# Kernel optimization log

Hardware: AMD Instinct MI355X
Metric: run time of the kernel (lower is better)

## Reference

```python
import jax, jax.numpy as jnp
import numpy as np

N_NODES = 20000
N_EDGES = 320000
NFEAT = 50
ALPHA = 0.2  # leaky relu slope
EPS = 1e-16


def _gat_head(x, src, dst, W, a, concat):
    # x: (N, Fin), W: (Fin, Fout), a: (2*Fout,)
    N = x.shape[0]
    Wh = x @ W                      # (N, Fout)
    Fout = W.shape[1]
    # edge_h @ a == Wh[src] @ a[:Fout] + Wh[dst] @ a[Fout:]
    s_src = Wh @ a[:Fout]           # (N,)
    s_dst = Wh @ a[Fout:]           # (N,)
    e = jax.nn.leaky_relu(s_src[src] + s_dst[dst], negative_slope=ALPHA)  # (E,)
    # segment softmax over incoming edges of each target node
    e_max = jax.ops.segment_max(e, dst, num_segments=N)   # (N,)
    e_exp = jnp.exp(e - e_max[dst])                         # (E,)
    e_sum = jax.ops.segment_sum(e_exp, dst, num_segments=N)
    att = e_exp / (e_sum[dst] + EPS)                        # (E,)
    msg = Wh[src] * att[:, None]                            # (E, Fout)
    h = jax.ops.segment_sum(msg, dst, num_segments=N)       # (N, Fout)
    return jax.nn.elu(h) if concat else h


def _multi_head(x, src, dst, W, a, concat):
    # W: (H, Fin, Fout), a: (H, 2*Fout) -> (H, N, Fout)
    return jax.vmap(_gat_head, in_axes=(None, None, None, 0, 0, None))(x, src, dst, W, a, concat)


def setup_inputs() -> dict:
    key = jax.random.key(0)
    ks = jax.random.split(key, 8)
    x = jax.random.normal(ks[0], (N_NODES, NFEAT), dtype=jnp.float32)
    edge_index = jax.random.randint(ks[1], (2, N_EDGES), 0, N_NODES, dtype=jnp.int64)
    s = 0.1
    W1 = jax.random.normal(ks[2], (4, NFEAT, 256), dtype=jnp.float32) * s
    a1 = jax.random.normal(ks[3], (4, 512), dtype=jnp.float32) * s
    W2 = jax.random.normal(ks[4], (4, 1024, 256), dtype=jnp.float32) * s
    a2 = jax.random.normal(ks[5], (4, 512), dtype=jnp.float32) * s
    W3 = jax.random.normal(ks[6], (6, 1024, 121), dtype=jnp.float32) * s
    a3 = jax.random.normal(ks[7], (6, 242), dtype=jnp.float32) * s
    return {"x": x, "edge_index": edge_index, "W1": W1, "a1": a1, "W2": W2, "a2": a2, "W3": W3, "a3": a3}


def reference(x, edge_index, W1, a1, W2, a2, W3, a3):
    src, dst = edge_index[0], edge_index[1]
    N = x.shape[0]
    # layer 1: 4 heads, concat -> (N, 1024), then elu
    h1 = _multi_head(x, src, dst, W1, a1, True)      # (4, N, 256)
    x1 = jnp.transpose(h1, (1, 0, 2)).reshape(N, -1)  # concat along feature dim
    x1 = jax.nn.elu(x1)
    # layer 2: 4 heads, concat + skip connection, then elu
    h2 = _multi_head(x1, src, dst, W2, a2, True)
    x2 = jnp.transpose(h2, (1, 0, 2)).reshape(N, -1)
    x2 = jax.nn.elu(x2 + x1)
    # layer 3: 6 heads, no concat-elu, mean over heads
    h3 = _multi_head(x2, src, dst, W3, a3, False)     # (6, N, 121)
    x3 = jnp.mean(h3, axis=0)
    return jax.nn.sigmoid(x3)
```

## Files before the change

### kernel.cpp

```cpp
#include <hip/hip_runtime.h>
#include <cstdint>

#define N_NODES 20000
#define N_EDGES 320000
#define ALPHA 0.2f
#define GAT_EPS 1e-16f
#define MPAD 20096
#define RBLK 157
#define RHI 20
#define SCAN_BLKS 80
#define BT_ROWS 1152

typedef __attribute__((ext_vector_type(8))) _Float16 half8;
typedef __attribute__((ext_vector_type(4))) _Float16 half4t;
typedef __attribute__((ext_vector_type(16))) float f32x16;
typedef __attribute__((ext_vector_type(2))) float f32x2;

__device__ __forceinline__ float elu1(float x) { return x > 0.f ? x : __expf(x) - 1.f; }

__device__ __forceinline__ unsigned char f2fp8(float x) {
    return (unsigned char)(__builtin_amdgcn_cvt_pk_fp8_f32(x, 0.f, 0, false) & 0xff);
}

__device__ __forceinline__ void async16(const void* g, void* l) {
    __builtin_amdgcn_global_load_lds(
        (const __attribute__((address_space(1))) unsigned int*)g,
        (__attribute__((address_space(3))) unsigned int*)l, 16, 0, 0);
}

__device__ __forceinline__ float rdlanef(float v, int j) {
    return __int_as_float(__builtin_amdgcn_readlane(__float_as_int(v), j));
}

template <bool HI>
__device__ __forceinline__ f32x2 cvt8(unsigned int u) {
    return __builtin_amdgcn_cvt_pk_f32_fp8((int)u, HI);
}

__global__ void hist_kernel(const int* __restrict__ dst, int* __restrict__ counts, int E) {
    int e = blockIdx.x * blockDim.x + threadIdx.x;
    if (e < E) atomicAdd(&counts[dst[e]], 1);
}

__global__ void scan1_kernel(const int* __restrict__ counts, int* __restrict__ excl,
                             int* __restrict__ partial, int N) {
    __shared__ int sh[256];
    int t = threadIdx.x, b = blockIdx.x;
    int i = b * 256 + t;
    int v = (i < N) ? counts[i] : 0;
    sh[t] = v;
    __syncthreads();
    for (int d = 1; d < 256; d <<= 1) {
        int x = (t >= d) ? sh[t - d] : 0;
        __syncthreads();
        sh[t] += x;
        __syncthreads();
    }
    if (i < N) excl[i] = sh[t] - v;
    if (t == 255) partial[b] = sh[255];
}

__global__ void scan2_kernel(int* __restrict__ partial) {
    __shared__ int sh[128];
    int t = threadIdx.x;
    int v = (t < SCAN_BLKS) ? partial[t] : 0;
    sh[t] = v;
    __syncthreads();
    for (int d = 1; d < 128; d <<= 1) {
        int x = (t >= d) ? sh[t - d] : 0;
        __syncthreads();
        sh[t] += x;
        __syncthreads();
    }
    if (t < SCAN_BLKS) partial[t] = sh[t] - v;
}

__global__ void scan3_kernel(const int* __restrict__ excl, const int* __restrict__ partial,
                             int* __restrict__ rowptr, int* __restrict__ cursor, int N, int E) {
    int t = threadIdx.x, b = blockIdx.x;
    int i = b * 256 + t;
    if (i < N) {
        int v = excl[i] + partial[b];
        rowptr[i] = v;
        cursor[i] = v;
    }
    if (i == 0) rowptr[N] = E;
}

__global__ void scatter_kernel(const int* __restrict__ src, const int* __restrict__ dst,
                               int* __restrict__ cursor, int* __restrict__ esrc, int E) {
    int e = blockIdx.x * blockDim.x + threadIdx.x;
    if (e < E) {
        int p = atomicAdd(&cursor[dst[e]], 1);
        esrc[p] = src[e];
    }
}

__global__ void pack_x16(const float* __restrict__ x, _Float16* __restrict__ A) {
    int idx = blockIdx.x * 256 + threadIdx.x;
    int r = idx >> 6, c = idx & 63;
    float v = (r < N_NODES && c < 50) ? x[r * 50 + c] : 0.f;
    A[idx] = (_Float16)v;
}

__global__ void pack_bt1(const float* __restrict__ W, _Float16* __restrict__ Bt) {
    int idx = blockIdx.x * 256 + threadIdx.x;
    int c = idx >> 6, k = idx & 63;
    int h = c >> 8, f = c & 255;
    float v = (k < 50) ? W[((size_t)h * 50 + k) * 256 + f] : 0.f;
    Bt[idx] = (_Float16)v;
}

__global__ void pack_bt16(const float* __restrict__ W, _Float16* __restrict__ Bt,
                          int F, int Fpad, int Ctot) {
    int c = blockIdx.y;
    int k = blockIdx.x * blockDim.x + threadIdx.x;
    float v = 0.f;
    if (c < Ctot) {
        int h = c / Fpad, f = c - h * Fpad;
        if (f < F) v = W[(size_t)h * 1024 * F + (size_t)k * F + f];
    }
    Bt[(size_t)c * 1024 + k] = (_Float16)v;
}

__global__ __launch_bounds__(64) void wtilde_kernel(const float* __restrict__ W,
                                                    const float* __restrict__ a,
                                                    _Float16* __restrict__ BT, int Kreal,
                                                    int Kdim, int F, int H, int Nfeat) {
    int k = blockIdx.x, j = blockIdx.y;
    if (j >= 2 * H) return;
    int lane = threadIdx.x;
    int h = j < H ? j : j - H;
    int ao = j < H ? 0 : F;
    float s = 0.f;
    if (k < Kreal) {
        const float* wp = W + ((size_t)h * Kreal + k) * F;
        const float* ap = a + (size_t)h * 2 * F + ao;
        for (int f = lane; f < F; f += 64) s += wp[f] * ap[f];
    }
#pragma unroll
    for (int off = 32; off; off >>= 1) s += __shfl_down(s, off);
    if (lane == 0) BT[(size_t)(Nfeat + j) * Kdim + k] = (_Float16)s;
}

__global__ __launch_bounds__(256) void gemm_f16(const _Float16* __restrict__ A,
                                                const _Float16* __restrict__ BT,
                                                unsigned char* __restrict__ C8,
                                                float* __restrict__ SPRE,
                                                int M, int Nfeat, int ld, int Kdim, int Cblk,
                                                int ldA, int mode) {
    int id = blockIdx.x;
    int xm = id & 7, q = id >> 3;
    int cb = q % Cblk, rh = q / Cblk;
    int rb = rh * 8 + xm;
    if (rb >= RBLK) return;
    __shared__ __align__(16) _Float16 sA[128 * 64];
    __shared__ __align__(16) _Float16 sB[128 * 64];
    int t = threadIdx.x;
    int row0 = rb * 128, col0 = cb * 128;
    int lane = t & 63, wave = t >> 6;
    int wm = wave >> 1, wn = wave & 1;
    int l31 = lane & 31;
    int lhi = lane >> 5;

    int koff = (mode == 1) ? ((cb >> 1) * 64) : 0;
    const _Float16* gA = A + (size_t)row0 * ldA + koff;
    const _Float16* gB = BT + (size_t)col0 * Kdim;

    int sR[4], sgl[4];
#pragma unroll
    for (int i = 0; i < 4; i++) {
        int m = i * 256 + t;
        sR[i] = m >> 3;
        sgl[i] = (m & 7) ^ (sR[i] & 7);
    }

    f32x16 acc[2][2] = {};

    for (int k0 = 0; k0 < Kdim; k0 += 64) {
        __syncthreads();
#pragma unroll
        for (int i = 0; i < 4; i++) {
            const _Float16* pa = gA + (size_t)sR[i] * ldA + k0 + sgl[i] * 8;
            const _Float16* pb = gB + (size_t)sR[i] * Kdim + k0 + sgl[i] * 8;
            async16(pa, sA + (i * 256 + t) * 8);
            async16(pb, sB + (i * 256 + t) * 8);
        }
        __syncthreads();
#pragma unroll
        for (int kk = 0; kk < 4; kk++) {
            int g = kk * 2 + lhi;
            half8 af[2], bf[2];
#pragma unroll
            for (int mt = 0; mt < 2; mt++) {
                int R = wm * 64 + mt * 32 + l31;
                int gp = g ^ (R & 7);
                af[mt] = *(const half8*)(sA + R * 64 + gp * 8);
            }
#pragma unroll
            for (int nt = 0; nt < 2; nt++) {
                int R = wn * 64 + nt * 32 + l31;
                int gp = g ^ (R & 7);
                bf[nt] = *(const half8*)(sB + R * 64 + gp * 8);
            }
#pragma unroll
            for (int mt = 0; mt < 2; mt++)
#pragma unroll
                for (int nt = 0; nt < 2; nt++)
                    acc[mt][nt] = __builtin_amdgcn_mfma_f32_32x32x16_f16(af[mt], bf[nt], acc[mt][nt], 0, 0, 0);
        }
    }

    int cb32 = col0 + wn * 64 + l31;
    int rb32 = row0 + wm * 64 + 4 * lhi;
    if (mode == 1) {
        _Float16* C16 = (_Float16*)C8;
#pragma unroll
        for (int mt = 0; mt < 2; mt++)
#pragma unroll
            for (int nt = 0; nt < 2; nt++) {
                int gc = cb32 + nt * 32;
                if (gc < Nfeat) {
#pragma unroll
                    for (int r = 0; r < 16; r++) {
                        int gr = rb32 + mt * 32 + (r & 3) + 8 * (r >> 2);
                        if (gr < M) C16[(size_t)gr * ld + gc] = (_Float16)elu1(elu1(acc[mt][nt][r]));
                    }
                }
            }
        return;
    }
#pragma unroll
    for (int mt = 0; mt < 2; mt++)
#pragma unroll
        for (int nt = 0; nt < 2; nt++) {
            int gc = cb32 + nt * 32;
            if (gc < Nfeat) {
#pragma unroll
                for (int r = 0; r < 16; r++) {
                    int gr = rb32 + mt * 32 + (r & 3) + 8 * (r >> 2);
                    if (gr < M) C8[(size_t)gr * ld + gc] = f2fp8(acc[mt][nt][r]);
                }
            } else if (gc < Nfeat + 12) {
                int j = gc - Nfeat;
#pragma unroll
                for (int r = 0; r < 16; r++) {
                    int gr = rb32 + mt * 32 + (r & 3) + 8 * (r >> 2);
                    if (gr < M) SPRE[(size_t)j * N_NODES + gr] = acc[mt][nt][r];
                }
            }
        }
}

__global__ __launch_bounds__(256) void aggx1_kernel(const int* __restrict__ rowptr,
                                                    const int* __restrict__ esrc,
                                                    const float* __restrict__ SPRE,
                                                    const _Float16* __restrict__ A1,
                                                    _Float16* __restrict__ XB, int N) {
    int wv = threadIdx.x >> 6;
    int lane = threadIdx.x & 63;
    int n = blockIdx.x * 4 + wv;
    if (n >= N) return;
    int start = rowptr[n], end = rowptr[n + 1];
    int cnt = end - start;
    float sd0 = SPRE[(size_t)4 * N + n];
    float sd1 = SPRE[(size_t)5 * N + n];
    float sd2 = SPRE[(size_t)6 * N + n];
    float sd3 = SPRE[(size_t)7 * N + n];
    const unsigned char* Wb = (const unsigned char*)A1 + 2 * lane;
    float acc0 = 0.f, acc1 = 0.f, acc2 = 0.f, acc3 = 0.f;

    if (cnt <= 64) {
        int e = start + lane;
        bool act = e < end;
        int idx = act ? esrc[e] : 0;
        float g0 = SPRE[idx];
        float g1 = SPRE[(size_t)N + idx];
        float g2 = SPRE[(size_t)2 * N + idx];
        float g3 = SPRE[(size_t)3 * N + idx];
        int voff = idx << 7;

        unsigned short wA[8], wB[8], wC[8], wD[8];
        auto ISSUE = [&](unsigned short (&buf)[8], int base) {
#pragma unroll
            for (int u = 0; u < 8; u++) {
                int off = __builtin_amdgcn_readlane(voff, base + u);
                buf[u] = *(const unsigned short*)(Wb + (unsigned)off);
            }
        };
        ISSUE(wA, 0);
        if (cnt > 8)  ISSUE(wB, 8);
        if (cnt > 16) ISSUE(wC, 16);
        if (cnt > 24) ISSUE(wD, 24);

        float sc0 = -1e30f, sc1 = -1e30f, sc2 = -1e30f, sc3 = -1e30f;
        if (act) {
            sc0 = g0 + sd0; sc0 = sc0 > 0.f ? sc0 : ALPHA * sc0;
            sc1 = g1 + sd1; sc1 = sc1 > 0.f ? sc1 : ALPHA * sc1;
            sc2 = g2 + sd2; sc2 = sc2 > 0.f ? sc2 : ALPHA * sc2;
            sc3 = g3 + sd3; sc3 = sc3 > 0.f ? sc3 : ALPHA * sc3;
        }
        float m0 = sc0, m1 = sc1, m2 = sc2, m3 = sc3;
#pragma unroll
        for (int off = 1; off < 64; off <<= 1) {
            m0 = fmaxf(m0, __shfl_xor(m0, off));
            m1 = fmaxf(m1, __shfl_xor(m1, off));
            m2 = fmaxf(m2, __shfl_xor(m2, off));
            m3 = fmaxf(m3, __shfl_xor(m3, off));
        }
        float p0 = act ? __expf(sc0 - m0) : 0.f;
        float p1 = act ? __expf(sc1 - m1) : 0.f;
        float p2 = act ? __expf(sc2 - m2) : 0.f;
        float p3 = act ? __expf(sc3 - m3) : 0.f;
        float s0 = p0, s1 = p1, s2 = p2, s3 = p3;
#pragma unroll
        for (int off = 1; off < 64; off <<= 1) {
            s0 += __shfl_xor(s0, off);
            s1 += __shfl_xor(s1, off);
            s2 += __shfl_xor(s2, off);
            s3 += __shfl_xor(s3, off);
        }
        p0 *= 1.f / (s0 + GAT_EPS);
        p1 *= 1.f / (s1 + GAT_EPS);
        p2 *= 1.f / (s2 + GAT_EPS);
        p3 *= 1.f / (s3 + GAT_EPS);

        auto CONSUME = [&](unsigned short (&buf)[8], int base) {
#pragma unroll
            for (int u = 0; u < 8; u++) {
                float xv = (float)(*(const _Float16*)&buf[u]);
                acc0 += rdlanef(p0, base + u) * xv;
                acc1 += rdlanef(p1, base + u) * xv;
                acc2 += rdlanef(p2, base + u) * xv;
                acc3 += rdlanef(p3, base + u) * xv;
            }
        };
        __builtin_amdgcn_s_setprio(1);
        CONSUME(wA, 0);
        if (cnt > 8)  { if (cnt > 32) ISSUE(wA, 32); CONSUME(wB, 8); }
        if (cnt > 16) { if (cnt > 40) ISSUE(wB, 40); CONSUME(wC, 16); }
        if (cnt > 24) { if (cnt > 48) ISSUE(wC, 48); CONSUME(wD, 24); }
        if (cnt > 32) { if (cnt > 56) ISSUE(wD, 56); CONSUME(wA, 32); }
        if (cnt > 40) CONSUME(wB, 40);
        if (cnt > 48) CONSUME(wC, 48);
        if (cnt > 56) CONSUME(wD, 56);
        __builtin_amdgcn_s_setprio(0);
    } else {
#pragma unroll
        for (int h = 0; h < 4; h++) {
            const float* ss = SPRE + (size_t)h * N;
            float sd = SPRE[(size_t)(4 + h) * N + n];
            float m = -1e30f, s = 0.f;
            for (int e0 = start; e0 < end; e0 += 64) {
                int e = e0 + lane;
                bool act = e < end;
                int idx = act ? esrc[e] : 0;
                float sc = -1e30f;
                if (act) {
                    sc = ss[idx] + sd;
                    sc = sc > 0.f ? sc : ALPHA * sc;
                }
                float mn = fmaxf(m, sc);
                s = s * __expf(m - mn) + (act ? __expf(sc - mn) : 0.f);
                m = mn;
            }
            float lm = m;
#pragma unroll
            for (int off = 1; off < 64; off <<= 1) m = fmaxf(m, __shfl_xor(m, off));
            float ptil = s * __expf(lm - m);
            s = ptil;
#pragma unroll
            for (int off = 1; off < 64; off <<= 1) s += __shfl_xor(s, off);
            float inv = 1.f / (s + GAT_EPS);
            float acch = 0.f;
            for (int e0 = start; e0 < end; e0 += 64) {
                int e = e0 + lane;
                bool act = e < end;
                int idx = act ? esrc[e] : 0;
                float sc = -1e30f;
                if (act) {
                    sc = ss[idx] + sd;
                    sc = sc > 0.f ? sc : ALPHA * sc;
                }
                float p = act ? __expf(sc - m) * inv : 0.f;
                int cn = end - e0; if (cn > 64) cn = 64;
                for (int j = 0; j < cn; j++) {
                    int ij = __builtin_amdgcn_readlane(idx, j);
                    float pj = rdlanef(p, j);
                    unsigned short w = *(const unsigned short*)(Wb + ((size_t)(unsigned)ij << 7));
                    acch += pj * (float)(*(const _Float16*)&w);
                }
            }
            if (h == 0) acc0 = acch;
            else if (h == 1) acc1 = acch;
            else if (h == 2) acc2 = acch;
            else acc3 = acch;
        }
    }

    size_t ob = (size_t)n * 256 + lane;
    XB[ob]       = (_Float16)acc0;
    XB[ob + 64]  = (_Float16)acc1;
    XB[ob + 128] = (_Float16)acc2;
    XB[ob + 192] = (_Float16)acc3;
}

__global__ __launch_bounds__(256) void attagg256_kernel(const int* __restrict__ rowptr,
                                                        const int* __restrict__ esrc,
                                                        const float* __restrict__ SPRE,
                                                        const unsigned char* __restrict__ WH8,
                                                        _Float16* __restrict__ X16,
                                                        int use_skip, int N) {
    int n = blockIdx.x;
    int h = threadIdx.x >> 6;
    int lane = threadIdx.x & 63;
    int start = rowptr[n], end = rowptr[n + 1];
    int cnt = end - start;
    const float* ss = SPRE + (size_t)h * N;
    float sd = SPRE[(size_t)(4 + h) * N + n];
    const unsigned char* Wb = WH8 + h * 256 + lane * 4;
    size_t o = (size_t)n * 1024 + h * 256 + lane * 4;
    half4t sk = {};
    if (use_skip) sk = *(const half4t*)(X16 + o);
    float a0 = 0.f, a1 = 0.f, a2 = 0.f, a3 = 0.f;

    if (cnt <= 64) {
        int e = start + lane;
        bool act = e < end;
        int idx = act ? esrc[e] : 0;
        float sv = ss[idx];

        unsigned int wA[8], wB[8], wC[8], wD[8];
        auto ISSUE = [&](unsigned int (&buf)[8], int base) {
#pragma unroll
            for (int u = 0; u < 8; u++) {
                int ij = __builtin_amdgcn_readlane(idx, base + u);
                buf[u] = *(const unsigned int*)(Wb + ((size_t)(unsigned)ij << 10));
            }
        };
        ISSUE(wA, 0);
        if (cnt > 8)  ISSUE(wB, 8);
        if (cnt > 16) ISSUE(wC, 16);
        if (cnt > 24) ISSUE(wD, 24);

        float sc = -1e30f;
        if (act) {
            sc = sv + sd;
            sc = sc > 0.f ? sc : ALPHA * sc;
        }
        float m = sc;
#pragma unroll
        for (int off = 1; off < 64; off <<= 1) m = fmaxf(m, __shfl_xor(m, off));
        float ptil = act ? __expf(sc - m) : 0.f;
        float s = ptil;
#pragma unroll
        for (int off = 1; off < 64; off <<= 1) s += __shfl_xor(s, off);
        float p = ptil * (1.f / (s + GAT_EPS));

        auto CONSUME = [&](unsigned int (&buf)[8], int base) {
#pragma unroll
            for (int u = 0; u < 8; u++) {
                float pj = rdlanef(p, base + u);
                f32x2 lo = cvt8<false>(buf[u]);
                f32x2 hi = cvt8<true>(buf[u]);
                a0 += pj * lo.x; a1 += pj * lo.y; a2 += pj * hi.x; a3 += pj * hi.y;
            }
        };
        __builtin_amdgcn_s_setprio(1);
        CONSUME(wA, 0);
        if (cnt > 8)  { if (cnt > 32) ISSUE(wA, 32); CONSUME(wB, 8); }
        if (cnt > 16) { if (cnt > 40) ISSUE(wB, 40); CONSUME(wC, 16); }
        if (cnt > 24) { if (cnt > 48) ISSUE(wC, 48); CONSUME(wD, 24); }
        if (cnt > 32) { if (cnt > 56) ISSUE(wD, 56); CONSUME(wA, 32); }
        if (cnt > 40) CONSUME(wB, 40);
        if (cnt > 48) CONSUME(wC, 48);
        if (cnt > 56) CONSUME(wD, 56);
        __builtin_amdgcn_s_setprio(0);
    } else {
        float m = -1e30f, s = 0.f;
        int sidx = 0; float ssc = -1e30f;
        for (int e0 = start; e0 < end; e0 += 64) {
            int e = e0 + lane;
            bool act = e < end;
            int idx = act ? esrc[e] : 0;
            float sc = -1e30f;
            if (act) {
                sc = ss[idx] + sd;
                sc = sc > 0.f ? sc : ALPHA * sc;
            }
            sidx = idx; ssc = sc;
            float mn = fmaxf(m, sc);
            s = s * __expf(m - mn) + (act ? __expf(sc - mn) : 0.f);
            m = mn;
        }
        float lm = m;
#pragma unroll
        for (int off = 1; off < 64; off <<= 1) m = fmaxf(m, __shfl_xor(m, off));
        float ptil = s * __expf(lm - m);
        s = ptil;
#pragma unroll
        for (int off = 1; off < 64; off <<= 1) s += __shfl_xor(s, off);
        float inv = 1.f / (s + GAT_EPS);

        int lastStart = start + (((end - start - 1) >> 6) << 6);
        for (int e0 = start; e0 < end; e0 += 64) {
            int e = e0 + lane;
            bool act = e < end;
            int idx; float p;
            if (e0 == lastStart) {
                idx = sidx;
                p = act ? __expf(ssc - m) * inv : 0.f;
            } else {
                idx = act ? esrc[e] : 0;
                float sc = -1e30f;
                if (act) {
                    sc = ss[idx] + sd;
                    sc = sc > 0.f ? sc : ALPHA * sc;
                }
                p = act ? __expf(sc - m) * inv : 0.f;
            }
            int cn = end - e0; if (cn > 64) cn = 64;
            for (int j = 0; j < cn; j++) {
                int ij = __builtin_amdgcn_readlane(idx, j);
                float pj = rdlanef(p, j);
                unsigned int w = *(const unsigned int*)(Wb + (size_t)ij * 1024);
                f32x2 lo = cvt8<false>(w);
                f32x2 hi = cvt8<true>(w);
                a0 += pj * lo.x; a1 += pj * lo.y; a2 += pj * hi.x; a3 += pj * hi.y;
            }
        }
    }

    float v0, v1, v2, v3;
    if (use_skip) {
        v0 = elu1(elu1(a0) + (float)sk.x);
        v1 = elu1(elu1(a1) + (float)sk.y);
        v2 = elu1(elu1(a2) + (float)sk.z);
        v3 = elu1(elu1(a3) + (float)sk.w);
    } else {
        v0 = elu1(elu1(a0)); v1 = elu1(elu1(a1));
        v2 = elu1(elu1(a2)); v3 = elu1(elu1(a3));
    }
    half4t r;
    r.x = (_Float16)v0; r.y = (_Float16)v1; r.z = (_Float16)v2; r.w = (_Float16)v3;
    *(half4t*)(X16 + o) = r;
}

__global__ __launch_bounds__(384) void attagg726_kernel(const int* __restrict__ rowptr,
                                                        const int* __restrict__ esrc,
                                                        const float* __restrict__ SPRE,
                                                        const unsigned char* __restrict__ WH8,
                                                        float* __restrict__ out, int N) {
    __shared__ float part[6][124];
    int n = blockIdx.x;
    int t = threadIdx.x;
    int h = t >> 6;
    int lane = t & 63;
    int start = rowptr[n], end = rowptr[n + 1];
    int cnt = end - start;
    const float* ss = SPRE + (size_t)h * N;
    float sd = SPRE[(size_t)(6 + h) * N + n];
    const unsigned char* Wb = WH8 + h * 124 + 2 * lane;
    float a0 = 0.f, a1 = 0.f;

    if (cnt <= 64) {
        int e = start + lane;
        bool act = e < end;
        int idx = act ? esrc[e] : 0;
        float sv = ss[idx];

        unsigned short wA[8], wB[8], wC[8], wD[8];
        auto ISSUE = [&](unsigned short (&buf)[8], int base) {
#pragma unroll
            for (int u = 0; u < 8; u++) {
                int ij = __builtin_amdgcn_readlane(idx, base + u);
                buf[u] = *(const unsigned short*)(Wb + (size_t)(unsigned)ij * 768u);
            }
        };
        ISSUE(wA, 0);
        if (cnt > 8)  ISSUE(wB, 8);
        if (cnt > 16) ISSUE(wC, 16);
        if (cnt > 24) ISSUE(wD, 24);

        float sc = -1e30f;
        if (act) {
            sc = sv + sd;
            sc = sc > 0.f ? sc : ALPHA * sc;
        }
        float m = sc;
#pragma unroll
        for (int off = 1; off < 64; off <<= 1) m = fmaxf(m, __shfl_xor(m, off));
        float ptil = act ? __expf(sc - m) : 0.f;
        float s = ptil;
#pragma unroll
        for (int off = 1; off < 64; off <<= 1) s += __shfl_xor(s, off);
        float p = ptil * (1.f / (s + GAT_EPS));

        auto CONSUME = [&](unsigned short (&buf)[8], int base) {
#pragma unroll
            for (int u = 0; u < 8; u++) {
                float pj = rdlanef(p, base + u);
                f32x2 f = cvt8<false>(buf[u]);
                a0 += pj * f.x; a1 += pj * f.y;
            }
        };
        __builtin_amdgcn_s_setprio(1);
        CONSUME(wA, 0);
        if (cnt > 8)  { if (cnt > 32) ISSUE(wA, 32); CONSUME(wB, 8); }
        if (cnt > 16) { if (cnt > 40) ISSUE(wB, 40); CONSUME(wC, 16); }
        if (cnt > 24) { if (cnt > 48) ISSUE(wC, 48); CONSUME(wD, 24); }
        if (cnt > 32) { if (cnt > 56) ISSUE(wD, 56); CONSUME(wA, 32); }
        if (cnt > 40) CONSUME(wB, 40);
        if (cnt > 48) CONSUME(wC, 48);
        if (cnt > 56) CONSUME(wD, 56);
        __builtin_amdgcn_s_setprio(0);
    } else {
        float m = -1e30f, s = 0.f;
        int sidx = 0; float ssc = -1e30f;
        for (int e0 = start; e0 < end; e0 += 64) {
            int e = e0 + lane;
            bool act = e < end;
            int idx = act ? esrc[e] : 0;
            float sc = -1e30f;
            if (act) {
                sc = ss[idx] + sd;
                sc = sc > 0.f ? sc : ALPHA * sc;
            }
            sidx = idx; ssc = sc;
            float mn = fmaxf(m, sc);
            s = s * __expf(m - mn) + (act ? __expf(sc - mn) : 0.f);
            m = mn;
        }
        float lm = m;
#pragma unroll
        for (int off = 1; off < 64; off <<= 1) m = fmaxf(m, __shfl_xor(m, off));
        float ptil = s * __expf(lm - m);
        s = ptil;
#pragma unroll
        for (int off = 1; off < 64; off <<= 1) s += __shfl_xor(s, off);
        float inv = 1.f / (s + GAT_EPS);

        int lastStart = start + (((end - start - 1) >> 6) << 6);
        for (int e0 = start; e0 < end; e0 += 64) {
            int e = e0 + lane;
            bool act = e < end;
            int idx; float p;
            if (e0 == lastStart) {
                idx = sidx;
                p = act ? __expf(ssc - m) * inv : 0.f;
            } else {
                idx = act ? esrc[e] : 0;
                float sc = -1e30f;
                if (act) {
                    sc = ss[idx] + sd;
                    sc = sc > 0.f ? sc : ALPHA * sc;
                }
                p = act ? __expf(sc - m) * inv : 0.f;
            }
            int cn = end - e0; if (cn > 64) cn = 64;
            if (lane < 62) {
                for (int j = 0; j < cn; j++) {
                    int ij = __builtin_amdgcn_readlane(idx, j);
                    float pj = rdlanef(p, j);
                    unsigned short w = *(const unsigned short*)(Wb + (size_t)ij * 768);
                    f32x2 f = cvt8<false>(w);
                    a0 += pj * f.x; a1 += pj * f.y;
                }
            }
        }
    }

    if (lane < 62) {
        part[h][2 * lane]     = a0;
        part[h][2 * lane + 1] = a1;
    }
    __syncthreads();
    if (t < 121) {
        float tot = (part[0][t] + part[1][t] + part[2][t] +
                     part[3][t] + part[4][t] + part[5][t]) * (1.f / 6.f);
        out[(size_t)n * 121 + t] = 1.f / (1.f + __expf(-tot));
    }
}

extern "C" void kernel_launch(void* const* d_in, const int* in_sizes, int n_in,
                              void* d_out, int out_size, void* d_ws, size_t ws_size,
                              hipStream_t stream) {
    const float* x  = (const float*)d_in[0];
    const int*   ei = (const int*)d_in[1];
    const float* W1 = (const float*)d_in[2];
    const float* a1 = (const float*)d_in[3];
    const float* W2 = (const float*)d_in[4];
    const float* a2 = (const float*)d_in[5];
    const float* W3 = (const float*)d_in[6];
    const float* a3 = (const float*)d_in[7];
    float* out = (float*)d_out;
    const int N = N_NODES, E = N_EDGES;
    const int* src = ei;
    const int* dst = ei + E;

    char* ws = (char*)d_ws;
    size_t off = 0;
    auto alloc = [&](size_t b) { size_t o = off; off += (b + 255) & ~(size_t)255; return o; };
    _Float16* X16  = (_Float16*)(ws + alloc((size_t)MPAD * 1024 * 2));
    unsigned char* WH8 = (unsigned char*)(ws + alloc((size_t)MPAD * 1024));
    _Float16* BT16 = (_Float16*)(ws + alloc((size_t)BT_ROWS * 1024 * 2));
    _Float16* A1   = (_Float16*)(ws + alloc((size_t)MPAD * 64 * 2));
    _Float16* BT1  = (_Float16*)(ws + alloc((size_t)BT_ROWS * 64 * 2));
    _Float16* XB   = (_Float16*)(ws + alloc((size_t)MPAD * 256 * 2));
    _Float16* BTS  = (_Float16*)(ws + alloc((size_t)128 * 64 * 2));
    float* SPRE   = (float*)(ws + alloc((size_t)12 * N * 4));
    int*   rowptr = (int*)(ws + alloc((size_t)(N + 1) * 4));
    int*   cursor = (int*)(ws + alloc((size_t)N * 4));
    int*   counts = (int*)(ws + alloc((size_t)N * 4));
    int*   excl   = (int*)(ws + alloc((size_t)N * 4));
    int*   partial= (int*)(ws + alloc((size_t)SCAN_BLKS * 4));
    int*   esrc   = (int*)(ws + alloc((size_t)E * 4));

    hipMemsetAsync(counts, 0, (size_t)N * 4, stream);
    hist_kernel<<<(E + 255) / 256, 256, 0, stream>>>(dst, counts, E);
    scan1_kernel<<<SCAN_BLKS, 256, 0, stream>>>(counts, excl, partial, N);
    scan2_kernel<<<1, 128, 0, stream>>>(partial);
    scan3_kernel<<<SCAN_BLKS, 256, 0, stream>>>(excl, partial, rowptr, cursor, N, E);
    scatter_kernel<<<(E + 255) / 256, 256, 0, stream>>>(src, dst, cursor, esrc, E);
    hipMemsetAsync(X16 + (size_t)N * 1024, 0, (size_t)(MPAD - N) * 1024 * 2, stream);
    hipMemsetAsync(XB + (size_t)N * 256, 0, (size_t)(MPAD - N) * 256 * 2, stream);

    pack_x16<<<MPAD * 64 / 256, 256, 0, stream>>>(x, A1);
    pack_bt1<<<1024 * 64 / 256, 256, 0, stream>>>(W1, BT1);
    wtilde_kernel<<<dim3(64, 8), 64, 0, stream>>>(W1, a1, BTS, 50, 64, 256, 4, 0);
    gemm_f16<<<8 * RHI * 1, 256, 0, stream>>>(A1, BTS, WH8, SPRE, N, 0, 1024, 64, 1, 64, 0);
    aggx1_kernel<<<(N + 3) / 4, 256, 0, stream>>>(rowptr, esrc, SPRE, A1, XB, N);
    gemm_f16<<<8 * RHI * 8, 256, 0, stream>>>(XB, BT1, (unsigned char*)X16, SPRE, N, 1024, 1024, 64, 8, 256, 1);

    pack_bt16<<<dim3(4, 1024), 256, 0, stream>>>(W2, BT16, 256, 256, 1024);
    wtilde_kernel<<<dim3(1024, 8), 64, 0, stream>>>(W2, a2, BT16, 1024, 1024, 256, 4, 1024);
    gemm_f16<<<8 * RHI * 9, 256, 0, stream>>>(X16, BT16, WH8, SPRE, N, 1024, 1024, 1024, 9, 1024, 0);
    attagg256_kernel<<<N, 256, 0, stream>>>(rowptr, esrc, SPRE, WH8, X16, 1, N);

    pack_bt16<<<dim3(4, 744), 256, 0, stream>>>(W3, BT16, 121, 124, 744);
    wtilde_kernel<<<dim3(1024, 12), 64, 0, stream>>>(W3, a3, BT16, 1024, 1024, 121, 6, 744);
    gemm_f16<<<8 * RHI * 6, 256, 0, stream>>>(X16, BT16, WH8, SPRE, N, 744, 768, 1024, 6, 1024, 0);
    attagg726_kernel<<<N, 384, 0, stream>>>(rowptr, esrc, SPRE, WH8, out, N);
}
```

Measured before the change: 408.6 us.

## Fold weight-packing kernels into graph kernels and merge scan passes

Weight packing and attention-vector folding (pack_x16, pack_bt1, pack_bt16, wtilde) now run as extra blocks appended to the histogram, layer-1 aggregation and layer-2 attention kernels. This removes separate launches and lets the independent weight prep overlap with graph work. The scan2 kernel is dropped; each scan3 block reduces the preceding partials itself. The cost is extra block-index branching and possible contention for resources inside the combined kernels.

```diff
diff --git a/kernel.cpp b/kernel.cpp
--- a/kernel.cpp
+++ b/kernel.cpp
@@ -11,6 +11,16 @@
 #define SCAN_BLKS 80
 #define BT_ROWS 1152
 
+#define HB1 1250
+#define PXB 5024
+#define PB1 256
+#define WT1B 128
+#define AGB 5000
+#define PL2 4096
+#define WT2B 2048
+#define PL3 2976
+#define WT3B 3072
+
 typedef __attribute__((ext_vector_type(8))) _Float16 half8;
 typedef __attribute__((ext_vector_type(4))) _Float16 half4t;
 typedef __attribute__((ext_vector_type(16))) float f32x16;
@@ -37,9 +47,62 @@
     return __builtin_amdgcn_cvt_pk_f32_fp8((int)u, HI);
 }
 
-__global__ void hist_kernel(const int* __restrict__ dst, int* __restrict__ counts, int E) {
-    int e = blockIdx.x * blockDim.x + threadIdx.x;
-    if (e < E) atomicAdd(&counts[dst[e]], 1);
+__device__ __forceinline__ void wtilde_pair(const float* __restrict__ W,
+                                            const float* __restrict__ a,
+                                            _Float16* __restrict__ BT,
+                                            int Kreal, int Kdim, int F, int H, int Nfeat,
+                                            int k, int j, int lane) {
+    int h = j < H ? j : j - H;
+    int ao = j < H ? 0 : F;
+    float s = 0.f;
+    if (k < Kreal) {
+        const float* wp = W + ((size_t)h * Kreal + k) * F;
+        const float* ap = a + (size_t)h * 2 * F + ao;
+        for (int f = lane; f < F; f += 64) s += wp[f] * ap[f];
+    }
+#pragma unroll
+    for (int off = 32; off; off >>= 1) s += __shfl_down(s, off);
+    if (lane == 0) BT[(size_t)(Nfeat + j) * Kdim + k] = (_Float16)s;
+}
+
+__device__ __forceinline__ void pack_bt16_body(const float* __restrict__ W,
+                                               _Float16* __restrict__ Bt,
+                                               int F, int Fpad, int Ctot, int c, int k) {
+    float v = 0.f;
+    if (c < Ctot) {
+        int h = c / Fpad, f = c - h * Fpad;
+        if (f < F) v = W[(size_t)h * 1024 * F + (size_t)k * F + f];
+    }
+    Bt[(size_t)c * 1024 + k] = (_Float16)v;
+}
+
+__global__ __launch_bounds__(256) void hist_plus(const int* __restrict__ dst,
+                                                 int* __restrict__ counts, int E,
+                                                 const float* __restrict__ x,
+                                                 _Float16* __restrict__ A1,
+                                                 const float* __restrict__ W1,
+                                                 _Float16* __restrict__ BT1,
+                                                 const float* __restrict__ a1,
+                                                 _Float16* __restrict__ BTS) {
+    int b = blockIdx.x, t = threadIdx.x;
+    if (b < HB1) {
+        int e = b * 256 + t;
+        if (e < E) atomicAdd(&counts[dst[e]], 1);
+    } else if (b < HB1 + PXB) {
+        int idx = (b - HB1) * 256 + t;
+        int r = idx >> 6, c = idx & 63;
+        float v = (r < N_NODES && c < 50) ? x[r * 50 + c] : 0.f;
+        A1[idx] = (_Float16)v;
+    } else if (b < HB1 + PXB + PB1) {
+        int idx = (b - HB1 - PXB) * 256 + t;
+        int c = idx >> 6, k = idx & 63;
+        int h = c >> 8, f = c & 255;
+        float v = (k < 50) ? W1[((size_t)h * 50 + k) * 256 + f] : 0.f;
+        BT1[idx] = (_Float16)v;
+    } else {
+        int p = (b - HB1 - PXB - PB1) * 4 + (t >> 6);
+        wtilde_pair(W1, a1, BTS, 50, 64, 256, 4, 0, p & 63, p >> 6, t & 63);
+    }
 }
 
 __global__ void scan1_kernel(const int* __restrict__ counts, int* __restrict__ excl,
@@ -60,29 +123,21 @@
     if (t == 255) partial[b] = sh[255];
 }
 
-__global__ void scan2_kernel(int* __restrict__ partial) {
-    __shared__ int sh[128];
-    int t = threadIdx.x;
-    int v = (t < SCAN_BLKS) ? partial[t] : 0;
-    sh[t] = v;
-    __syncthreads();
-    for (int d = 1; d < 128; d <<= 1) {
-        int x = (t >= d) ? sh[t - d] : 0;
-        __syncthreads();
-        sh[t] += x;
-        __syncthreads();
-    }
-    if (t < SCAN_BLKS) partial[t] = sh[t] - v;
-}
-
 __global__ void scan3_kernel(const int* __restrict__ excl, const int* __restrict__ partial,
                              int* __restrict__ rowptr, int* __restrict__ cursor, int N, int E) {
+    __shared__ int wsum[4];
     int t = threadIdx.x, b = blockIdx.x;
+    int v = (t < SCAN_BLKS && t < b) ? partial[t] : 0;
+#pragma unroll
+    for (int off = 32; off; off >>= 1) v += __shfl_down(v, off);
+    if ((t & 63) == 0) wsum[t >> 6] = v;
+    __syncthreads();
+    int base = wsum[0] + wsum[1] + wsum[2] + wsum[3];
     int i = b * 256 + t;
     if (i < N) {
-        int v = excl[i] + partial[b];
-        rowptr[i] = v;
-        cursor[i] = v;
+        int val = excl[i] + base;
+        rowptr[i] = val;
+        cursor[i] = val;
     }
     if (i == 0) rowptr[N] = E;
 }
@@ -94,53 +149,6 @@
         int p = atomicAdd(&cursor[dst[e]], 1);
         esrc[p] = src[e];
     }
-}
-
-__global__ void pack_x16(const float* __restrict__ x, _Float16* __restrict__ A) {
-    int idx = blockIdx.x * 256 + threadIdx.x;
-    int r = idx >> 6, c = idx & 63;
-    float v = (r < N_NODES && c < 50) ? x[r * 50 + c] : 0.f;
-    A[idx] = (_Float16)v;
-}
-
-__global__ void pack_bt1(const float* __restrict__ W, _Float16* __restrict__ Bt) {
-    int idx = blockIdx.x * 256 + threadIdx.x;
-    int c = idx >> 6, k = idx & 63;
-    int h = c >> 8, f = c & 255;
-    float v = (k < 50) ? W[((size_t)h * 50 + k) * 256 + f] : 0.f;
-    Bt[idx] = (_Float16)v;
-}
-
-__global__ void pack_bt16(const float* __restrict__ W, _Float16* __restrict__ Bt,
-                          int F, int Fpad, int Ctot) {
-    int c = blockIdx.y;
-    int k = blockIdx.x * blockDim.x + threadIdx.x;
-    float v = 0.f;
-    if (c < Ctot) {
-        int h = c / Fpad, f = c - h * Fpad;
-        if (f < F) v = W[(size_t)h * 1024 * F + (size_t)k * F + f];
-    }
-    Bt[(size_t)c * 1024 + k] = (_Float16)v;
-}
-
-__global__ __launch_bounds__(64) void wtilde_kernel(const float* __restrict__ W,
-                                                    const float* __restrict__ a,
-                                                    _Float16* __restrict__ BT, int Kreal,
-                                                    int Kdim, int F, int H, int Nfeat) {
-    int k = blockIdx.x, j = blockIdx.y;
-    if (j >= 2 * H) return;
-    int lane = threadIdx.x;
-    int h = j < H ? j : j - H;
-    int ao = j < H ? 0 : F;
-    float s = 0.f;
-    if (k < Kreal) {
-        const float* wp = W + ((size_t)h * Kreal + k) * F;
-        const float* ap = a + (size_t)h * 2 * F + ao;
-        for (int f = lane; f < F; f += 64) s += wp[f] * ap[f];
-    }
-#pragma unroll
-    for (int off = 32; off; off >>= 1) s += __shfl_down(s, off);
-    if (lane == 0) BT[(size_t)(Nfeat + j) * Kdim + k] = (_Float16)s;
 }
 
 __global__ __launch_bounds__(256) void gemm_f16(const _Float16* __restrict__ A,
@@ -252,14 +260,28 @@
         }
 }
 
-__global__ __launch_bounds__(256) void aggx1_kernel(const int* __restrict__ rowptr,
-                                                    const int* __restrict__ esrc,
-                                                    const float* __restrict__ SPRE,
-                                                    const _Float16* __restrict__ A1,
-                                                    _Float16* __restrict__ XB, int N) {
+__global__ __launch_bounds__(256) void aggx1_plus(const int* __restrict__ rowptr,
+                                                  const int* __restrict__ esrc,
+                                                  const float* __restrict__ SPRE,
+                                                  const _Float16* __restrict__ A1,
+                                                  _Float16* __restrict__ XB, int N,
+                                                  const float* __restrict__ W2,
+                                                  const float* __restrict__ a2,
+                                                  _Float16* __restrict__ BT16) {
+    int bid = blockIdx.x;
     int wv = threadIdx.x >> 6;
     int lane = threadIdx.x & 63;
-    int n = blockIdx.x * 4 + wv;
+    if (bid >= AGB) {
+        if (bid < AGB + PL2) {
+            int pb = bid - AGB;
+            pack_bt16_body(W2, BT16, 256, 256, 1024, pb >> 2, (pb & 3) * 256 + threadIdx.x);
+        } else {
+            int p = (bid - AGB - PL2) * 4 + wv;
+            wtilde_pair(W2, a2, BT16, 1024, 1024, 256, 4, 1024, p & 1023, p >> 10, lane);
+        }
+        return;
+    }
+    int n = bid * 4 + wv;
     if (n >= N) return;
     int start = rowptr[n], end = rowptr[n + 1];
     int cnt = end - start;
@@ -405,15 +427,29 @@
     XB[ob + 192] = (_Float16)acc3;
 }
 
-__global__ __launch_bounds__(256) void attagg256_kernel(const int* __restrict__ rowptr,
-                                                        const int* __restrict__ esrc,
-                                                        const float* __restrict__ SPRE,
-                                                        const unsigned char* __restrict__ WH8,
-                                                        _Float16* __restrict__ X16,
-                                                        int use_skip, int N) {
-    int n = blockIdx.x;
+__global__ __launch_bounds__(256) void attagg256_plus(const int* __restrict__ rowptr,
+                                                      const int* __restrict__ esrc,
+                                                      const float* __restrict__ SPRE,
+                                                      const unsigned char* __restrict__ WH8,
+                                                      _Float16* __restrict__ X16,
+                                                      int use_skip, int N,
+                                                      const float* __restrict__ W3,
+                                                      const float* __restrict__ a3,
+                                                      _Float16* __restrict__ BT16) {
+    int bid = blockIdx.x;
     int h = threadIdx.x >> 6;
     int lane = threadIdx.x & 63;
+    if (bid >= N_NODES) {
+        if (bid < N_NODES + PL3) {
+            int pb = bid - N_NODES;
+            pack_bt16_body(W3, BT16, 121, 124, 744, pb >> 2, (pb & 3) * 256 + threadIdx.x);
+        } else {
+            int p = (bid - N_NODES - PL3) * 4 + h;
+            wtilde_pair(W3, a3, BT16, 1024, 1024, 121, 6, 744, p & 1023, p >> 10, lane);
+        }
+        return;
+    }
+    int n = bid;
     int start = rowptr[n], end = rowptr[n + 1];
     int cnt = end - start;
     const float* ss = SPRE + (size_t)h * N;
@@ -422,7 +458,7 @@
     size_t o = (size_t)n * 1024 + h * 256 + lane * 4;
     half4t sk = {};
     if (use_skip) sk = *(const half4t*)(X16 + o);
-    float a0 = 0.f, a1 = 0.f, a2 = 0.f, a3 = 0.f;
+    float a0 = 0.f, a1 = 0.f, a2 = 0.f, a3v = 0.f;
 
     if (cnt <= 64) {
         int e = start + lane;
@@ -463,7 +499,7 @@
                 float pj = rdlanef(p, base + u);
                 f32x2 lo = cvt8<false>(buf[u]);
                 f32x2 hi = cvt8<true>(buf[u]);
-                a0 += pj * lo.x; a1 += pj * lo.y; a2 += pj * hi.x; a3 += pj * hi.y;
+                a0 += pj * lo.x; a1 += pj * lo.y; a2 += pj * hi.x; a3v += pj * hi.y;
             }
         };
         __builtin_amdgcn_s_setprio(1);
@@ -526,7 +562,7 @@
                 unsigned int w = *(const unsigned int*)(Wb + (size_t)ij * 1024);
                 f32x2 lo = cvt8<false>(w);
                 f32x2 hi = cvt8<true>(w);
-                a0 += pj * lo.x; a1 += pj * lo.y; a2 += pj * hi.x; a3 += pj * hi.y;
+                a0 += pj * lo.x; a1 += pj * lo.y; a2 += pj * hi.x; a3v += pj * hi.y;
             }
         }
     }
@@ -536,10 +572,10 @@
         v0 = elu1(elu1(a0) + (float)sk.x);
         v1 = elu1(elu1(a1) + (float)sk.y);
         v2 = elu1(elu1(a2) + (float)sk.z);
-        v3 = elu1(elu1(a3) + (float)sk.w);
+        v3 = elu1(elu1(a3v) + (float)sk.w);
     } else {
         v0 = elu1(elu1(a0)); v1 = elu1(elu1(a1));
-        v2 = elu1(elu1(a2)); v3 = elu1(elu1(a3));
+        v2 = elu1(elu1(a2)); v3 = elu1(elu1(a3v));
     }
     half4t r;
     r.x = (_Float16)v0; r.y = (_Float16)v1; r.z = (_Float16)v2; r.w = (_Float16)v3;
@@ -717,28 +753,20 @@
     int*   esrc   = (int*)(ws + alloc((size_t)E * 4));
 
     hipMemsetAsync(counts, 0, (size_t)N * 4, stream);
-    hist_kernel<<<(E + 255) / 256, 256, 0, stream>>>(dst, counts, E);
+    hist_plus<<<HB1 + PXB + PB1 + WT1B, 256, 0, stream>>>(dst, counts, E, x, A1, W1, BT1, a1, BTS);
     scan1_kernel<<<SCAN_BLKS, 256, 0, stream>>>(counts, excl, partial, N);
-    scan2_kernel<<<1, 128, 0, stream>>>(partial);
     scan3_kernel<<<SCAN_BLKS, 256, 0, stream>>>(excl, partial, rowptr, cursor, N, E);
     scatter_kernel<<<(E + 255) / 256, 256, 0, stream>>>(src, dst, cursor, esrc, E);
     hipMemsetAsync(X16 + (size_t)N * 1024, 0, (size_t)(MPAD - N) * 1024 * 2, stream);
     hipMemsetAsync(XB + (size_t)N * 256, 0, (size_t)(MPAD - N) * 256 * 2, stream);
 
-    pack_x16<<<MPAD * 64 / 256, 256, 0, stream>>>(x, A1);
-    pack_bt1<<<1024 * 64 / 256, 256, 0, stream>>>(W1, BT1);
-    wtilde_kernel<<<dim3(64, 8), 64, 0, stream>>>(W1, a1, BTS, 50, 64, 256, 4, 0);
     gemm_f16<<<8 * RHI * 1, 256, 0, stream>>>(A1, BTS, WH8, SPRE, N, 0, 1024, 64, 1, 64, 0);
-    aggx1_kernel<<<(N + 3) / 4, 256, 0, stream>>>(rowptr, esrc, SPRE, A1, XB, N);
+    aggx1_plus<<<AGB + PL2 + WT2B, 256, 0, stream>>>(rowptr, esrc, SPRE, A1, XB, N, W2, a2, BT16);
     gemm_f16<<<8 * RHI * 8, 256, 0, stream>>>(XB, BT1, (unsigned char*)X16, SPRE, N, 1024, 1024, 64, 8, 256, 1);
 
-    pack_bt16<<<dim3(4, 1024), 256, 0, stream>>>(W2, BT16, 256, 256, 1024);
-    wtilde_kernel<<<dim3(1024, 8), 64, 0, stream>>>(W2, a2, BT16, 1024, 1024, 256, 4, 1024);
     gemm_f16<<<8 * RHI * 9, 256, 0, stream>>>(X16, BT16, WH8, SPRE, N, 1024, 1024, 1024, 9, 1024, 0);
-    attagg256_kernel<<<N, 256, 0, stream>>>(rowptr, esrc, SPRE, WH8, X16, 1, N);
-
-    pack_bt16<<<dim3(4, 744), 256, 0, stream>>>(W3, BT16, 121, 124, 744);
-    wtilde_kernel<<<dim3(1024, 12), 64, 0, stream>>>(W3, a3, BT16, 1024, 1024, 121, 6, 744);
+    attagg256_plus<<<N_NODES + PL3 + WT3B, 256, 0, stream>>>(rowptr, esrc, SPRE, WH8, X16, 1, N, W3, a3, BT16);
+
     gemm_f16<<<8 * RHI * 6, 256, 0, stream>>>(X16, BT16, WH8, SPRE, N, 744, 768, 1024, 6, 1024, 0);
     attagg726_kernel<<<N, 384, 0, stream>>>(rowptr, esrc, SPRE, WH8, out, N);
 }
```

Result: no change. 404.0 us (-1.1%).
